# Kernel optimization log

Measured on AMD Instinct MI355X. Metric: run time of the kernel, lower is better.

## Reference

```python
import jax, jax.numpy as jnp
import numpy as np

EPS = 1e-5  # torch LayerNorm default


def _score_branch(feat, g, b, W1, B1, W2, B2):
    # feat: [B, C, H, W] -> tokens [B, H*W, C]
    B, C, H, Wd = feat.shape
    tokens = jnp.transpose(feat, (0, 2, 3, 1)).reshape(B, H * Wd, C)
    mu = tokens.mean(-1, keepdims=True)
    var = jnp.mean(jnp.square(tokens - mu), axis=-1, keepdims=True)
    x = (tokens - mu) * jax.lax.rsqrt(var + EPS) * g + b
    h = jax.nn.gelu(jnp.einsum('btc,cd->btd', x, W1) + B1, approximate=False)
    s = jax.nn.sigmoid(jnp.einsum('btd,do->bto', h, W2) + B2)  # [B, HW, 1]
    return s.reshape(B, 1, H, Wd)


def setup_inputs() -> dict:
    key = jax.random.key(0)
    ks = jax.random.split(key, 6)
    M, B, C, H, W = 3, 16, 768, 48, 48
    Ch = C // 4
    return {
        'feat0': jax.random.normal(ks[0], (B, C, H, W), jnp.float32),
        'feat1': jax.random.normal(ks[1], (B, C, H, W), jnp.float32),
        'feat2': jax.random.normal(ks[2], (B, C, H, W), jnp.float32),
        'ln_g': jnp.ones((M, C), jnp.float32),
        'ln_b': jnp.zeros((M, C), jnp.float32),
        'w1': jax.random.normal(ks[3], (M, C, Ch), jnp.float32) * 0.02,
        'b1': jnp.zeros((M, Ch), jnp.float32),
        'w2': jax.random.normal(ks[4], (M, Ch, 1), jnp.float32) * 0.02,
        'b2': jnp.zeros((M, 1), jnp.float32),
    }


def reference(feat0, feat1, feat2, ln_g, ln_b, w1, b1, w2, b2):
    feats = (feat0, feat1, feat2)
    outs = []
    for i, feat in enumerate(feats):  # fixed small loop over modalities
        outs.append(_score_branch(feat, ln_g[i], ln_b[i], w1[i], b1[i], w2[i], b2[i]))
    return tuple(outs)
```

## Files before the change

### kernel.cpp

```cpp
#include <hip/hip_runtime.h>
#include <hip/hip_bf16.h>

typedef __attribute__((ext_vector_type(8))) short bf16x8;
typedef __attribute__((ext_vector_type(4))) short bf16x4;
typedef __attribute__((ext_vector_type(4))) float f32x4;

__device__ __forceinline__ unsigned short f2bf(float f) {
    __hip_bfloat16 h = __float2bfloat16(f);
    return __builtin_bit_cast(unsigned short, h);
}

#define BT 64
#define TPM 576
#define NCHUNK 24

__global__ void prep_partial(const float* __restrict__ w1, const float* __restrict__ lng,
                             const float* __restrict__ lnb,
                             float* __restrict__ upart, float* __restrict__ vpart)
{
    const int m   = blockIdx.x >> 3;
    const int seg = blockIdx.x & 7;
    const int d   = threadIdx.x;
    const float* w1m = w1 + (size_t)m * 768 * 192;
    const float* gm  = lng + m * 768;
    const float* bm  = lnb + m * 768;
    const int c0 = seg * 96;
    float su = 0.f, sv = 0.f;
    for (int c = 0; c < 96; ++c) {
        float wv = w1m[(size_t)(c0 + c) * 192 + d];
        su += gm[c0 + c] * wv;
        sv += bm[c0 + c] * wv;
    }
    upart[(m * 8 + seg) * 192 + d] = su;
    vpart[(m * 8 + seg) * 192 + d] = sv;
}

__global__ void prep_combine(const float* __restrict__ upart, const float* __restrict__ vpart,
                             const float* __restrict__ b1,
                             float* __restrict__ u, float* __restrict__ vb)
{
    const int m = blockIdx.x;
    const int d = threadIdx.x;
    float su = 0.f, sv = 0.f;
    for (int s = 0; s < 8; ++s) {
        su += upart[(m * 8 + s) * 192 + d];
        sv += vpart[(m * 8 + s) * 192 + d];
    }
    u[m * 192 + d]  = su;
    vb[m * 192 + d] = sv + b1[m * 192 + d];
}

__global__ void prep_pack(const float* __restrict__ w1, const float* __restrict__ lng,
                          unsigned short* __restrict__ w1f)
{
    const int m  = blockIdx.x / 24;
    const int kk = blockIdx.x % 24;
    const int tid = threadIdx.x;
    __shared__ float ws[32 * 192];
    const float* w1m = w1 + ((size_t)m * 768 + kk * 32) * 192;
    const float* gm  = lng + m * 768 + kk * 32;
    for (int i = tid; i < 6144; i += 256) {
        int cl = i / 192, d = i % 192;
        ws[i] = gm[cl] * w1m[(size_t)cl * 192 + d];
    }
    __syncthreads();
    unsigned short* outp = w1f + ((size_t)m * 24 + kk) * 6144;
    for (int i = tid; i < 6144; i += 256) {
        int nf   = i >> 9;
        int rem  = i & 511;
        int lane = rem >> 3;
        int j    = rem & 7;
        int cl   = ((lane >> 4) << 3) + j;
        int d    = (nf << 4) + (lane & 15);
        outp[i]  = f2bf(ws[cl * 192 + d]);
    }
}

__global__ __launch_bounds__(256, 3)
void fused_main(const float* __restrict__ f0, const float* __restrict__ f1,
                const float* __restrict__ f2,
                const unsigned short* __restrict__ w1f,
                const float* __restrict__ u_g, const float* __restrict__ vb_g,
                const float* __restrict__ w2_g, const float* __restrict__ b2_g,
                float* __restrict__ out)
{
    const int bx   = blockIdx.x;
    const int mod  = bx / TPM;
    const int tile = bx % TPM;
    const float* feat = (mod == 0) ? f0 : ((mod == 1) ? f1 : f2);
    const int T0   = tile * BT;
    const int bimg = T0 / 2304;
    const int hw0  = T0 % 2304;
    const float* fbase = feat + (size_t)bimg * 768 * 2304 + hw0;

    const int tid = threadIdx.x;
    const int l   = tid & 63;
    const int w   = tid >> 6;
    const int p   = l & 31;
    const int cg  = l >> 5;

    __shared__ unsigned short Atile[2][64][40];
    __shared__ float redS[4][64], redQ[4][64];
    __shared__ float mu_s[64], rs_s[64];
    __shared__ float red2[4][64];

    const unsigned short* w1fm = w1f + (size_t)mod * 24 * 6144;

    f32x4 acc[4][3];
    #pragma unroll
    for (int a = 0; a < 4; ++a)
        #pragma unroll
        for (int b = 0; b < 3; ++b) acc[a][b] = (f32x4){0.f, 0.f, 0.f, 0.f};

    float sum0 = 0.f, ssq0 = 0.f, sum1 = 0.f, ssq1 = 0.f;

    float2 avA[4], avB[4];
    bf16x8 bfA[3], bfB[3];

    auto LOADA = [&](float2 (&av)[4], int kk) {
        const float* sA = fbase + (size_t)(kk * 32 + w * 8 + cg * 4) * 2304 + 2 * p;
        #pragma unroll
        for (int j = 0; j < 4; ++j)
            av[j] = *reinterpret_cast<const float2*>(sA + (size_t)j * 2304);
    };
    auto LOADB = [&](bf16x8 (&bf)[3], int kk) {
        const bf16x8* sB = reinterpret_cast<const bf16x8*>(w1fm + (size_t)kk * 6144);
        #pragma unroll
        for (int nf = 0; nf < 3; ++nf)
            bf[nf] = sB[(w * 3 + nf) * 64 + l];
    };

    auto STEP = [&](float2 (&av)[4], bf16x8 (&bf)[3], int kk) {
        const int buf = kk & 1;
        const int t0 = 2 * p, t1 = t0 + 1;
        const int s0 = w ^ (((t0 >> 2) ^ (t0 >> 4)) & 3);
        const int s1 = w ^ (((t1 >> 2) ^ (t1 >> 4)) & 3);
        bf16x4 q0, q1;
        #pragma unroll
        for (int j = 0; j < 4; ++j) {
            float x0 = av[j].x, x1 = av[j].y;
            q0[j] = (short)f2bf(x0);
            q1[j] = (short)f2bf(x1);
            sum0 += x0; ssq0 += x0 * x0;
            sum1 += x1; ssq1 += x1 * x1;
        }
        *reinterpret_cast<bf16x4*>(&Atile[buf][t0][s0 * 8 + cg * 4]) = q0;
        *reinterpret_cast<bf16x4*>(&Atile[buf][t1][s1 * 8 + cg * 4]) = q1;
        int kn = kk + 2; if (kn > NCHUNK - 1) kn = NCHUNK - 1;
        LOADA(av, kn);
        asm volatile("s_waitcnt lgkmcnt(0)" ::: "memory");
        __builtin_amdgcn_sched_barrier(0);
        __builtin_amdgcn_s_barrier();
        const int col = l & 15, lg = l >> 4;
        #pragma unroll
        for (int mf = 0; mf < 4; ++mf) {
            int t = mf * 16 + col;
            int s = lg ^ (((t >> 2) ^ (t >> 4)) & 3);
            bf16x8 af = *reinterpret_cast<const bf16x8*>(&Atile[buf][t][s * 8]);
            #pragma unroll
            for (int nf = 0; nf < 3; ++nf)
                acc[mf][nf] = __builtin_amdgcn_mfma_f32_16x16x32_bf16(
                                  af, bf[nf], acc[mf][nf], 0, 0, 0);
        }
        LOADB(bf, kn);
    };

    LOADA(avA, 0); LOADB(bfA, 0);
    LOADA(avB, 1); LOADB(bfB, 1);
    #pragma unroll 1
    for (int kt = 0; kt < NCHUNK / 2; ++kt) {
        STEP(avA, bfA, 2 * kt);
        STEP(avB, bfB, 2 * kt + 1);
    }

    sum0 += __shfl_xor(sum0, 32);  sum1 += __shfl_xor(sum1, 32);
    ssq0 += __shfl_xor(ssq0, 32);  ssq1 += __shfl_xor(ssq1, 32);
    if (l < 32) {
        redS[w][2 * p] = sum0;  redS[w][2 * p + 1] = sum1;
        redQ[w][2 * p] = ssq0;  redQ[w][2 * p + 1] = ssq1;
    }
    __syncthreads();
    if (tid < 64) {
        float S = redS[0][tid] + redS[1][tid] + redS[2][tid] + redS[3][tid];
        float Q = redQ[0][tid] + redQ[1][tid] + redQ[2][tid] + redQ[3][tid];
        float mu = S * (1.f / 768.f);
        float var = Q * (1.f / 768.f) - mu * mu;
        mu_s[tid] = mu;
        rs_s[tid] = rsqrtf(var + 1e-5f);
    }
    __syncthreads();

    const int col = l & 15, lg = l >> 4;
    const float* um  = u_g  + mod * 192;
    const float* vbm = vb_g + mod * 192;
    const float* w2m = w2_g + mod * 192;
    float uf[3], vbf[3], w2f[3];
    #pragma unroll
    for (int nf = 0; nf < 3; ++nf) {
        int d = (w * 3 + nf) * 16 + col;
        uf[nf] = um[d]; vbf[nf] = vbm[d]; w2f[nf] = w2m[d];
    }
    float ps[4][4];
    #pragma unroll
    for (int mf = 0; mf < 4; ++mf) {
        #pragma unroll
        for (int r = 0; r < 4; ++r) {
            int t = mf * 16 + lg * 4 + r;
            float mu = mu_s[t], rs = rs_s[t];
            float pp = 0.f;
            #pragma unroll
            for (int nf = 0; nf < 3; ++nf) {
                float x = rs * (acc[mf][nf][r] - mu * uf[nf]) + vbf[nf];
                float h = 0.5f * x * (1.f + erff(x * 0.70710678118f));
                pp += h * w2f[nf];
            }
            ps[mf][r] = pp;
        }
    }
    #pragma unroll
    for (int m = 1; m < 16; m <<= 1)
        #pragma unroll
        for (int mf = 0; mf < 4; ++mf)
            #pragma unroll
            for (int r = 0; r < 4; ++r)
                ps[mf][r] += __shfl_xor(ps[mf][r], m, 64);
    if (col == 0) {
        #pragma unroll
        for (int mf = 0; mf < 4; ++mf)
            #pragma unroll
            for (int r = 0; r < 4; ++r)
                red2[w][mf * 16 + lg * 4 + r] = ps[mf][r];
    }
    __syncthreads();
    if (tid < 64) {
        float logit = red2[0][tid] + red2[1][tid] + red2[2][tid] + red2[3][tid] + b2_g[mod];
        out[(size_t)mod * 36864 + T0 + tid] = 1.f / (1.f + expf(-logit));
    }
}

extern "C" void kernel_launch(void* const* d_in, const int* in_sizes, int n_in,
                              void* d_out, int out_size, void* d_ws, size_t ws_size,
                              hipStream_t stream)
{
    const float* f0  = (const float*)d_in[0];
    const float* f1  = (const float*)d_in[1];
    const float* f2  = (const float*)d_in[2];
    const float* lng = (const float*)d_in[3];
    const float* lnb = (const float*)d_in[4];
    const float* w1  = (const float*)d_in[5];
    const float* b1  = (const float*)d_in[6];
    const float* w2  = (const float*)d_in[7];
    const float* b2  = (const float*)d_in[8];
    float* out = (float*)d_out;

    char* ws = (char*)d_ws;
    unsigned short* w1f = (unsigned short*)ws;
    float* u     = (float*)(ws + 884736);
    float* vb    = (float*)(ws + 887040);
    float* upart = (float*)(ws + 889344);
    float* vpart = (float*)(ws + 907776);

    prep_partial<<<dim3(24), dim3(192), 0, stream>>>(w1, lng, lnb, upart, vpart);
    prep_combine<<<dim3(3),  dim3(192), 0, stream>>>(upart, vpart, b1, u, vb);
    prep_pack   <<<dim3(72), dim3(256), 0, stream>>>(w1, lng, w1f);
    fused_main  <<<dim3(3 * TPM), dim3(256), 0, stream>>>(f0, f1, f2, w1f, u, vb, w2, b2, out);
}
```

Baseline: 106.1 us.

## Merge prep kernels, remap block order, single-buffer B fragments, raise occupancy

The three weight-preparation kernels become one launch: 72 blocks pack W1 to bf16 and 3 blocks compute the u and vb vectors with a full serial reduction, which removes two launches and the partial buffers. The main kernel remaps block indices so consecutive blocks spread across modalities and tiles, raises launch bounds to 4 waves per SIMD, and uses a single B-fragment register buffer prefetched one chunk ahead instead of two. A-fragment loads are batched ahead of the MFMAs and redundant tail prefetches are skipped. The aim is lower launch overhead and more occupancy through lower register pressure, at the risk of exposing B-load latency and making the three-block u/vb reduction the slow part of the prep launch.

Measured after the change: 167.9 us. 58.2% more time.

```diff
diff --git a/kernel.cpp b/kernel.cpp
--- a/kernel.cpp
+++ b/kernel.cpp
@@ -9,74 +9,63 @@
     __hip_bfloat16 h = __float2bfloat16(f);
     return __builtin_bit_cast(unsigned short, h);
 }
+__device__ __forceinline__ void waitlgkm0() {
+    asm volatile("s_waitcnt lgkmcnt(0)" ::: "memory");
+}
 
 #define BT 64
 #define TPM 576
 #define NCHUNK 24
 
-__global__ void prep_partial(const float* __restrict__ w1, const float* __restrict__ lng,
-                             const float* __restrict__ lnb,
-                             float* __restrict__ upart, float* __restrict__ vpart)
+__global__ void prep_all(const float* __restrict__ w1, const float* __restrict__ lng,
+                         const float* __restrict__ lnb, const float* __restrict__ b1,
+                         unsigned short* __restrict__ w1f,
+                         float* __restrict__ u, float* __restrict__ vb)
 {
-    const int m   = blockIdx.x >> 3;
-    const int seg = blockIdx.x & 7;
-    const int d   = threadIdx.x;
-    const float* w1m = w1 + (size_t)m * 768 * 192;
-    const float* gm  = lng + m * 768;
-    const float* bm  = lnb + m * 768;
-    const int c0 = seg * 96;
-    float su = 0.f, sv = 0.f;
-    for (int c = 0; c < 96; ++c) {
-        float wv = w1m[(size_t)(c0 + c) * 192 + d];
-        su += gm[c0 + c] * wv;
-        sv += bm[c0 + c] * wv;
-    }
-    upart[(m * 8 + seg) * 192 + d] = su;
-    vpart[(m * 8 + seg) * 192 + d] = sv;
-}
-
-__global__ void prep_combine(const float* __restrict__ upart, const float* __restrict__ vpart,
-                             const float* __restrict__ b1,
-                             float* __restrict__ u, float* __restrict__ vb)
-{
-    const int m = blockIdx.x;
-    const int d = threadIdx.x;
-    float su = 0.f, sv = 0.f;
-    for (int s = 0; s < 8; ++s) {
-        su += upart[(m * 8 + s) * 192 + d];
-        sv += vpart[(m * 8 + s) * 192 + d];
-    }
-    u[m * 192 + d]  = su;
-    vb[m * 192 + d] = sv + b1[m * 192 + d];
-}
-
-__global__ void prep_pack(const float* __restrict__ w1, const float* __restrict__ lng,
-                          unsigned short* __restrict__ w1f)
-{
-    const int m  = blockIdx.x / 24;
-    const int kk = blockIdx.x % 24;
+    const int b   = blockIdx.x;
     const int tid = threadIdx.x;
-    __shared__ float ws[32 * 192];
-    const float* w1m = w1 + ((size_t)m * 768 + kk * 32) * 192;
-    const float* gm  = lng + m * 768 + kk * 32;
-    for (int i = tid; i < 6144; i += 256) {
-        int cl = i / 192, d = i % 192;
-        ws[i] = gm[cl] * w1m[(size_t)cl * 192 + d];
-    }
-    __syncthreads();
-    unsigned short* outp = w1f + ((size_t)m * 24 + kk) * 6144;
-    for (int i = tid; i < 6144; i += 256) {
-        int nf   = i >> 9;
-        int rem  = i & 511;
-        int lane = rem >> 3;
-        int j    = rem & 7;
-        int cl   = ((lane >> 4) << 3) + j;
-        int d    = (nf << 4) + (lane & 15);
-        outp[i]  = f2bf(ws[cl * 192 + d]);
-    }
-}
-
-__global__ __launch_bounds__(256, 3)
+    if (b < 72) {
+        const int m  = b / 24;
+        const int kk = b % 24;
+        __shared__ float ws[32 * 192];
+        const float* w1m = w1 + ((size_t)m * 768 + kk * 32) * 192;
+        const float* gm  = lng + m * 768 + kk * 32;
+        for (int i = tid; i < 6144; i += 256) {
+            int cl = i / 192, d = i % 192;
+            ws[i] = gm[cl] * w1m[(size_t)cl * 192 + d];
+        }
+        __syncthreads();
+        unsigned short* outp = w1f + ((size_t)m * 24 + kk) * 6144;
+        for (int i = tid; i < 6144; i += 256) {
+            int nf   = i >> 9;
+            int rem  = i & 511;
+            int lane = rem >> 3;
+            int j    = rem & 7;
+            int cl   = ((lane >> 4) << 3) + j;
+            int d    = (nf << 4) + (lane & 15);
+            outp[i]  = f2bf(ws[cl * 192 + d]);
+        }
+    } else {
+        const int m = b - 72;
+        if (tid < 192) {
+            const int d = tid;
+            const float* w1m = w1 + (size_t)m * 768 * 192;
+            const float* gm  = lng + m * 768;
+            const float* bm  = lnb + m * 768;
+            float su = 0.f, sv = 0.f;
+            #pragma unroll 16
+            for (int c = 0; c < 768; ++c) {
+                float wv = w1m[(size_t)c * 192 + d];
+                su += gm[c] * wv;
+                sv += bm[c] * wv;
+            }
+            u[m * 192 + d]  = su;
+            vb[m * 192 + d] = sv + b1[m * 192 + d];
+        }
+    }
+}
+
+__global__ __launch_bounds__(256, 4)
 void fused_main(const float* __restrict__ f0, const float* __restrict__ f1,
                 const float* __restrict__ f2,
                 const unsigned short* __restrict__ w1f,
@@ -84,7 +73,8 @@
                 const float* __restrict__ w2_g, const float* __restrict__ b2_g,
                 float* __restrict__ out)
 {
-    const int bx   = blockIdx.x;
+    const int bx0  = blockIdx.x;
+    const int bx   = (bx0 & 7) * 216 + (bx0 >> 3);
     const int mod  = bx / TPM;
     const int tile = bx % TPM;
     const float* feat = (mod == 0) ? f0 : ((mod == 1) ? f1 : f2);
@@ -98,6 +88,7 @@
     const int w   = tid >> 6;
     const int p   = l & 31;
     const int cg  = l >> 5;
+    const int col = l & 15, lg = l >> 4;
 
     __shared__ unsigned short Atile[2][64][40];
     __shared__ float redS[4][64], redQ[4][64];
@@ -115,7 +106,7 @@
     float sum0 = 0.f, ssq0 = 0.f, sum1 = 0.f, ssq1 = 0.f;
 
     float2 avA[4], avB[4];
-    bf16x8 bfA[3], bfB[3];
+    bf16x8 bf[3];
 
     auto LOADA = [&](float2 (&av)[4], int kk) {
         const float* sA = fbase + (size_t)(kk * 32 + w * 8 + cg * 4) * 2304 + 2 * p;
@@ -123,14 +114,14 @@
         for (int j = 0; j < 4; ++j)
             av[j] = *reinterpret_cast<const float2*>(sA + (size_t)j * 2304);
     };
-    auto LOADB = [&](bf16x8 (&bf)[3], int kk) {
+    auto LOADB = [&](int kk) {
         const bf16x8* sB = reinterpret_cast<const bf16x8*>(w1fm + (size_t)kk * 6144);
         #pragma unroll
         for (int nf = 0; nf < 3; ++nf)
             bf[nf] = sB[(w * 3 + nf) * 64 + l];
     };
 
-    auto STEP = [&](float2 (&av)[4], bf16x8 (&bf)[3], int kk) {
+    auto STEP = [&](float2 (&av)[4], int kk) {
         const int buf = kk & 1;
         const int t0 = 2 * p, t1 = t0 + 1;
         const int s0 = w ^ (((t0 >> 2) ^ (t0 >> 4)) & 3);
@@ -141,36 +132,39 @@
             float x0 = av[j].x, x1 = av[j].y;
             q0[j] = (short)f2bf(x0);
             q1[j] = (short)f2bf(x1);
-            sum0 += x0; ssq0 += x0 * x0;
-            sum1 += x1; ssq1 += x1 * x1;
+            sum0 += x0; ssq0 = fmaf(x0, x0, ssq0);
+            sum1 += x1; ssq1 = fmaf(x1, x1, ssq1);
         }
         *reinterpret_cast<bf16x4*>(&Atile[buf][t0][s0 * 8 + cg * 4]) = q0;
         *reinterpret_cast<bf16x4*>(&Atile[buf][t1][s1 * 8 + cg * 4]) = q1;
-        int kn = kk + 2; if (kn > NCHUNK - 1) kn = NCHUNK - 1;
-        LOADA(av, kn);
-        asm volatile("s_waitcnt lgkmcnt(0)" ::: "memory");
+        if (kk < NCHUNK - 2) LOADA(av, kk + 2);
+        waitlgkm0();
         __builtin_amdgcn_sched_barrier(0);
         __builtin_amdgcn_s_barrier();
-        const int col = l & 15, lg = l >> 4;
+        __builtin_amdgcn_sched_barrier(0);
+        bf16x8 af[4];
         #pragma unroll
         for (int mf = 0; mf < 4; ++mf) {
             int t = mf * 16 + col;
             int s = lg ^ (((t >> 2) ^ (t >> 4)) & 3);
-            bf16x8 af = *reinterpret_cast<const bf16x8*>(&Atile[buf][t][s * 8]);
+            af[mf] = *reinterpret_cast<const bf16x8*>(&Atile[buf][t][s * 8]);
+        }
+        #pragma unroll
+        for (int mf = 0; mf < 4; ++mf)
             #pragma unroll
             for (int nf = 0; nf < 3; ++nf)
                 acc[mf][nf] = __builtin_amdgcn_mfma_f32_16x16x32_bf16(
-                                  af, bf[nf], acc[mf][nf], 0, 0, 0);
-        }
-        LOADB(bf, kn);
+                                  af[mf], bf[nf], acc[mf][nf], 0, 0, 0);
+        if (kk < NCHUNK - 1) LOADB(kk + 1);
     };
 
-    LOADA(avA, 0); LOADB(bfA, 0);
-    LOADA(avB, 1); LOADB(bfB, 1);
+    LOADA(avA, 0);
+    LOADA(avB, 1);
+    LOADB(0);
     #pragma unroll 1
     for (int kt = 0; kt < NCHUNK / 2; ++kt) {
-        STEP(avA, bfA, 2 * kt);
-        STEP(avB, bfB, 2 * kt + 1);
+        STEP(avA, 2 * kt);
+        STEP(avB, 2 * kt + 1);
     }
 
     sum0 += __shfl_xor(sum0, 32);  sum1 += __shfl_xor(sum1, 32);
@@ -190,7 +184,6 @@
     }
     __syncthreads();
 
-    const int col = l & 15, lg = l >> 4;
     const float* um  = u_g  + mod * 192;
     const float* vbm = vb_g + mod * 192;
     const float* w2m = w2_g + mod * 192;
@@ -257,11 +250,7 @@
     unsigned short* w1f = (unsigned short*)ws;
     float* u     = (float*)(ws + 884736);
     float* vb    = (float*)(ws + 887040);
-    float* upart = (float*)(ws + 889344);
-    float* vpart = (float*)(ws + 907776);
-
-    prep_partial<<<dim3(24), dim3(192), 0, stream>>>(w1, lng, lnb, upart, vpart);
-    prep_combine<<<dim3(3),  dim3(192), 0, stream>>>(upart, vpart, b1, u, vb);
-    prep_pack   <<<dim3(72), dim3(256), 0, stream>>>(w1, lng, w1f);
-    fused_main  <<<dim3(3 * TPM), dim3(256), 0, stream>>>(f0, f1, f2, w1f, u, vb, w2, b2, out);
-}
+
+    prep_all  <<<dim3(75), dim3(256), 0, stream>>>(w1, lng, lnb, b1, w1f, u, vb);
+    fused_main<<<dim3(3 * TPM), dim3(256), 0, stream>>>(f0, f1, f2, w1f, u, vb, w2, b2, out);
+}
```
